# Performance work log

Measured on AMD Instinct MI355X. Metric: run time of the kernel, lower is better.

The kernel has to match this reference:

```python
import jax, jax.numpy as jnp
import numpy as np

NUM_EMBEDDINGS = 8192
EMBEDDING_DIM = 256
COMMITMENT_WEIGHT = 0.25
EMA_DECAY = 0.99
EPSILON = 1e-05


def setup_inputs() -> dict:
    key = jax.random.key(0)
    k1, k2 = jax.random.split(key)
    z = jax.random.normal(k1, (8, 4096, EMBEDDING_DIM), dtype=jnp.float32)
    # xavier-uniform-ish codebook init
    limit = np.sqrt(6.0 / (NUM_EMBEDDINGS + EMBEDDING_DIM))
    embeddings = jax.random.uniform(
        k2, (NUM_EMBEDDINGS, EMBEDDING_DIM), dtype=jnp.float32,
        minval=-limit, maxval=limit)
    ema_cluster_size = jnp.zeros((NUM_EMBEDDINGS,), dtype=jnp.float32)
    ema_embed_sum = embeddings.copy()
    return {
        'z': z,
        'embeddings': embeddings,
        'ema_cluster_size': ema_cluster_size,
        'ema_embed_sum': ema_embed_sum,
    }


def reference(z, embeddings, ema_cluster_size, ema_embed_sum):
    input_shape = z.shape
    D = input_shape[-1]
    z_flat = z.reshape(-1, D)                                  # [N, D]

    # Squared euclidean distances via expansion: ||z||^2 + ||e||^2 - 2 z.e
    z_sq = jnp.sum(z_flat * z_flat, axis=1, keepdims=True)     # [N, 1]
    e_sq = jnp.sum(embeddings * embeddings, axis=1)            # [K]
    ze = jnp.matmul(z_flat, embeddings.T)                      # [N, K]
    distances = z_sq + e_sq - 2.0 * ze                          # [N, K]
    indices = jnp.argmin(distances, axis=1)                    # [N] int

    z_q_flat = embeddings[indices]                             # [N, D] gather
    z_q = z_q_flat.reshape(input_shape)

    # commitment loss = mse(stop_grad(z_q), z)
    diff = jax.lax.stop_gradient(z_q) - z
    commitment_loss = jnp.mean(diff * diff) * COMMITMENT_WEIGHT

    # straight-through estimator
    z_q_st = z + jax.lax.stop_gradient(z_q - z)

    # EMA codebook update (functional version of the in-place buffer update)
    ones = jnp.ones_like(indices, dtype=embeddings.dtype)
    cluster_size = jax.ops.segment_sum(ones, indices, num_segments=NUM_EMBEDDINGS)
    embed_sum = jax.ops.segment_sum(z_flat, indices, num_segments=NUM_EMBEDDINGS)
    new_ema_cluster_size = EMA_DECAY * ema_cluster_size + (1.0 - EMA_DECAY) * cluster_size
    new_ema_embed_sum = EMA_DECAY * ema_embed_sum + (1.0 - EMA_DECAY) * embed_sum
    new_embeddings = new_ema_embed_sum / (new_ema_cluster_size[:, None] + EPSILON)

    indices_out = indices.reshape(input_shape[:-1])
    return (z_q_st, indices_out, commitment_loss,
            new_embeddings, new_ema_cluster_size, new_ema_embed_sum)
```

## Files before the change

### kernel.cpp

```cpp
#include <hip/hip_runtime.h>
#include <hip/hip_bf16.h>
#include <math.h>

#define N_TOK   32768
#define DIM     256
#define KC      8192

#define OUT_ZQ    0
#define OUT_IDX   8388608
#define OUT_LOSS  8421376
#define OUT_NEMB  8421377
#define OUT_CS    10518529
#define OUT_SUM   10526721

#define MARGIN  5e-3f
#define FLAGCAP 8192

typedef __attribute__((ext_vector_type(8))) __bf16 bf16x8;
typedef __attribute__((ext_vector_type(4))) float f32x4;

__device__ __forceinline__ void gload16(const void* g, void* l) {
  __builtin_amdgcn_global_load_lds((const __attribute__((address_space(1))) void*)g,
                                   (__attribute__((address_space(3))) void*)l, 16, 0, 0);
}

__device__ __forceinline__ float np_sumsq256(const float* __restrict__ p, int lane) {
  const int l = lane & 15;
  const int h = l >> 3;
  const int j = l & 7;
  const float* a = p + h * 128 + j;
  float x = a[0];
  float r = __fmul_rn(x, x);
  #pragma unroll
  for (int i = 1; i < 16; ++i) {
    x = a[8 * i];
    r = __fadd_rn(r, __fmul_rn(x, x));
  }
  r = __fadd_rn(r, __shfl_down(r, 1));
  r = __fadd_rn(r, __shfl_down(r, 2));
  r = __fadd_rn(r, __shfl_down(r, 4));
  float hi = __shfl(r, (lane & 48) | 8);
  return __fadd_rn(r, hi);
}

__global__ void vq_prep(const float* __restrict__ emb, float* __restrict__ esq,
                        short* __restrict__ esp2) {
  const int t = threadIdx.x;
  const int code = blockIdx.x * 8 + (t >> 5);
  const int p = t & 31, j = p >> 2, g = p & 3;
  const float* src = emb + (size_t)code * DIM + j * 32 + g * 8;
  const float4 v0 = *(const float4*)src;
  const float4 v1 = *(const float4*)(src + 4);
  const float xf[8] = {v0.x, v0.y, v0.z, v0.w, v1.x, v1.y, v1.z, v1.w};
  bf16x8 hb;
  #pragma unroll
  for (int e = 0; e < 8; ++e) hb[e] = (__bf16)xf[e];
  const int c = code & 15, sub = (code >> 4) & 3, ct = code >> 6;
  const int slot = (g + (c >> 1)) & 3;
  char* dst = (char*)esp2 + (size_t)ct * 32768 + ((sub * 8 + j) << 10) + c * 64 + slot * 16;
  *(bf16x8*)dst = hb;
  if (t < 128) {
    const int code2 = blockIdx.x * 8 + (t >> 4);
    const float s = np_sumsq256(emb + (size_t)code2 * DIM, t & 63);
    if ((t & 15) == 0) esq[code2] = s;
  }
}

__global__ void vq_transpose(const float* __restrict__ emb, float* __restrict__ embT) {
  __shared__ float t[64][65];
  const int tid = threadIdx.x;
  const int bc  = blockIdx.x & 127;
  const int bk  = blockIdx.x >> 7;
  const int cc0 = bc << 6, kc0 = bk << 6;
  const int col = tid & 63, qr = tid >> 6;
  #pragma unroll
  for (int i = 0; i < 16; ++i) {
    const int row = i * 4 + qr;
    t[row][col] = emb[(size_t)(cc0 + row) * DIM + kc0 + col];
  }
  __syncthreads();
  #pragma unroll
  for (int i = 0; i < 16; ++i) {
    const int krow = i * 4 + qr;
    embT[(size_t)(kc0 + krow) * KC + cc0 + col] = t[col][krow];
  }
}

__global__ void vq_init(int* __restrict__ hist, int* __restrict__ cnt) {
  const int i = blockIdx.x * blockDim.x + threadIdx.x;
  hist[i] = 0;
  if (i == 0) cnt[0] = 0;
}

__launch_bounds__(256, 2)
__global__ void vq_mfma(const float* __restrict__ z,
                        const short* __restrict__ esp,
                        const float* __restrict__ esq,
                        float* __restrict__ pb1,
                        int* __restrict__ pi1,
                        float* __restrict__ pb2) {
  __shared__ __align__(16) char lds[65536];
  const int tid  = threadIdx.x;
  const int lane = tid & 63;
  const int w    = tid >> 6;
  const int l15  = lane & 15;
  const int g    = lane >> 4;
  const int rt   = blockIdx.x >> 1;
  const int kh   = blockIdx.x & 1;
  const int row0 = rt * 128 + w * 32;
  const int ct0  = kh * 64, ct1 = ct0 + 64;
  const int gx   = (g + (l15 >> 1)) & 3;
  const char* espb = (const char*)esp;

#define STAGE(CT, BUFB)                                                          \
  {                                                                              \
    _Pragma("unroll")                                                            \
    for (int q_ = 0; q_ < 8; ++q_) {                                             \
      const int so_ = (((w << 3) + q_) << 10) + (lane << 4);                     \
      gload16(espb + (size_t)(CT) * 32768 + so_,                                 \
              (void*)(lds + (BUFB) + (((w << 3) + q_) << 10)));                  \
    }                                                                            \
  }

  STAGE(ct0, 0);

  bf16x8 Ahi[2][8], Alo[2][8];
  #pragma unroll
  for (int s = 0; s < 2; ++s) {
    const float* zr = z + (size_t)(row0 + s * 16 + l15) * DIM + g * 8;
    #pragma unroll
    for (int c = 0; c < 8; ++c) {
      const float4 v0 = *(const float4*)(zr + c * 32);
      const float4 v1 = *(const float4*)(zr + c * 32 + 4);
      const float xf[8] = {v0.x, v0.y, v0.z, v0.w, v1.x, v1.y, v1.z, v1.w};
      #pragma unroll
      for (int e = 0; e < 8; ++e) {
        __bf16 hb = (__bf16)xf[e];
        Ahi[s][c][e] = hb;
        Alo[s][c][e] = (__bf16)(xf[e] - (float)hb);
      }
    }
  }

  __syncthreads();

  float b1[2][4], b2[2][4];
  int   i1[2][4];
  #pragma unroll
  for (int s = 0; s < 2; ++s)
    #pragma unroll
    for (int r = 0; r < 4; ++r) { b1[s][r] = 3.4e38f; b2[s][r] = 3.4e38f; i1[s][r] = 0x7fffffff; }

#define COMP(BUFB)                                                                    \
  {                                                                                   \
    _Pragma("unroll")                                                                 \
    for (int j_ = 0; j_ < 8; ++j_) {                                                  \
      const char* bq_ = lds + (BUFB) + (j_ << 10) + (l15 << 6) + (gx << 4);           \
      const bf16x8 bF0 = *(const bf16x8*)(bq_);                                       \
      const bf16x8 bF1 = *(const bf16x8*)(bq_ + 8192);                                \
      const bf16x8 bF2 = *(const bf16x8*)(bq_ + 16384);                               \
      const bf16x8 bF3 = *(const bf16x8*)(bq_ + 24576);                               \
      acc[0][0] = __builtin_amdgcn_mfma_f32_16x16x32_bf16(Ahi[0][j_], bF0, acc[0][0], 0, 0, 0); \
      acc[0][1] = __builtin_amdgcn_mfma_f32_16x16x32_bf16(Ahi[0][j_], bF1, acc[0][1], 0, 0, 0); \
      acc[0][2] = __builtin_amdgcn_mfma_f32_16x16x32_bf16(Ahi[0][j_], bF2, acc[0][2], 0, 0, 0); \
      acc[0][3] = __builtin_amdgcn_mfma_f32_16x16x32_bf16(Ahi[0][j_], bF3, acc[0][3], 0, 0, 0); \
      acc[1][0] = __builtin_amdgcn_mfma_f32_16x16x32_bf16(Ahi[1][j_], bF0, acc[1][0], 0, 0, 0); \
      acc[1][1] = __builtin_amdgcn_mfma_f32_16x16x32_bf16(Ahi[1][j_], bF1, acc[1][1], 0, 0, 0); \
      acc[1][2] = __builtin_amdgcn_mfma_f32_16x16x32_bf16(Ahi[1][j_], bF2, acc[1][2], 0, 0, 0); \
      acc[1][3] = __builtin_amdgcn_mfma_f32_16x16x32_bf16(Ahi[1][j_], bF3, acc[1][3], 0, 0, 0); \
      acc[0][0] = __builtin_amdgcn_mfma_f32_16x16x32_bf16(Alo[0][j_], bF0, acc[0][0], 0, 0, 0); \
      acc[0][1] = __builtin_amdgcn_mfma_f32_16x16x32_bf16(Alo[0][j_], bF1, acc[0][1], 0, 0, 0); \
      acc[0][2] = __builtin_amdgcn_mfma_f32_16x16x32_bf16(Alo[0][j_], bF2, acc[0][2], 0, 0, 0); \
      acc[0][3] = __builtin_amdgcn_mfma_f32_16x16x32_bf16(Alo[0][j_], bF3, acc[0][3], 0, 0, 0); \
      acc[1][0] = __builtin_amdgcn_mfma_f32_16x16x32_bf16(Alo[1][j_], bF0, acc[1][0], 0, 0, 0); \
      acc[1][1] = __builtin_amdgcn_mfma_f32_16x16x32_bf16(Alo[1][j_], bF1, acc[1][1], 0, 0, 0); \
      acc[1][2] = __builtin_amdgcn_mfma_f32_16x16x32_bf16(Alo[1][j_], bF2, acc[1][2], 0, 0, 0); \
      acc[1][3] = __builtin_amdgcn_mfma_f32_16x16x32_bf16(Alo[1][j_], bF3, acc[1][3], 0, 0, 0); \
    }                                                                                 \
  }

  int bp = 0;
  for (int ct = ct0; ct < ct1; ++ct) {
    if (ct + 1 < ct1) STAGE(ct + 1, (bp ^ 1) << 15);

    float eqv[4];
    #pragma unroll
    for (int sub = 0; sub < 4; ++sub) eqv[sub] = esq[(ct << 6) + sub * 16 + l15];

    f32x4 acc[2][4];
    #pragma unroll
    for (int s = 0; s < 2; ++s)
      #pragma unroll
      for (int sub = 0; sub < 4; ++sub) acc[s][sub] = (f32x4){0.f, 0.f, 0.f, 0.f};

    COMP(bp << 15);

    #pragma unroll
    for (int s = 0; s < 2; ++s) {
      #pragma unroll
      for (int sub = 0; sub < 4; ++sub) {
        const int codeS = (ct << 6) + sub * 16 + l15;
        #pragma unroll
        for (int r = 0; r < 4; ++r) {
          const float sc = fmaf(-2.f, acc[s][sub][r], eqv[sub]);
          const bool lt = sc < b1[s][r];
          b2[s][r] = fminf(b2[s][r], fmaxf(sc, b1[s][r]));
          i1[s][r] = lt ? codeS : i1[s][r];
          b1[s][r] = fminf(b1[s][r], sc);
        }
      }
    }
    __syncthreads();
    bp ^= 1;
  }

  #pragma unroll
  for (int s = 0; s < 2; ++s) {
    #pragma unroll
    for (int r = 0; r < 4; ++r) {
      float v1 = b1[s][r], v2 = b2[s][r];
      int   j1 = i1[s][r];
      #pragma unroll
      for (int off = 1; off < 16; off <<= 1) {
        const float o1 = __shfl_xor(v1, off);
        const int   oj = __shfl_xor(j1, off);
        const float o2 = __shfl_xor(v2, off);
        v2 = fminf(fminf(v2, o2), fmaxf(v1, o1));
        const bool tk = (o1 < v1) || (o1 == v1 && oj < j1);
        j1 = tk ? oj : j1;
        v1 = fminf(v1, o1);
      }
      if (l15 == 0) {
        const int rr = kh * N_TOK + row0 + s * 16 + (g << 2) + r;
        pb1[rr] = v1; pi1[rr] = j1; pb2[rr] = v2;
      }
    }
  }
}

__global__ void vq_merge(const float* __restrict__ pb1, const int* __restrict__ pi1,
                         const float* __restrict__ pb2, int* __restrict__ idxf,
                         int* __restrict__ flag, int* __restrict__ cnt) {
  const int gi = blockIdx.x * blockDim.x + threadIdx.x;
  const float va = pb1[gi],        vb = pb1[N_TOK + gi];
  const int   ia = pi1[gi],        ib = pi1[N_TOK + gi];
  const float v2a = pb2[gi],       v2b = pb2[N_TOK + gi];
  float v1, v2; int i1;
  if (va < vb || (va == vb && ia < ib)) { v1 = va; i1 = ia; v2 = fminf(v2a, vb); }
  else                                  { v1 = vb; i1 = ib; v2 = fminf(v2b, va); }
  idxf[gi] = i1;
  if (v2 - v1 < MARGIN) {
    const int p = atomicAdd(cnt, 1);
    if (p < FLAGCAP) flag[p] = gi;
  }
}

__global__ void vq_rescan2(const float* __restrict__ z,
                           const float* __restrict__ embT,
                           const float* __restrict__ esq,
                           const int* __restrict__ flag,
                           const int* __restrict__ cnt,
                           float* __restrict__ rpv,
                           int* __restrict__ rpi) {
  __shared__ __align__(16) float zT[DIM][16];
  __shared__ float zsq_sh[16];
  __shared__ float rv[4][16];
  __shared__ int   ri[4][16];
  __shared__ int   rown[16];
  int n = *cnt; if (n > FLAGCAP) n = FLAGCAP;
  const int tid = threadIdx.x;
  const int lane = tid & 63, wv = tid >> 6;
  const int nb = (n + 15) >> 4;
  const int ntask = nb * 8;
  for (int task = blockIdx.x; task < ntask; task += gridDim.x) {
    const int bb = task >> 3, cz = task & 7;
    __syncthreads();
    if (tid < 16) rown[tid] = flag[min(bb * 16 + tid, n - 1)];
    __syncthreads();
    #pragma unroll
    for (int rr = 0; rr < 16; ++rr) zT[tid][rr] = z[(size_t)rown[rr] * DIM + tid];
    {
      const int rr = tid >> 4;
      const float s = np_sumsq256(z + (size_t)rown[rr] * DIM, lane);
      if ((tid & 15) == 0) zsq_sh[rr] = s;
    }
    __syncthreads();

    float a[16][4];
    #pragma unroll
    for (int rr = 0; rr < 16; ++rr)
      #pragma unroll
      for (int q = 0; q < 4; ++q) a[rr][q] = 0.f;

    const int c0 = cz * 1024 + tid;
    #pragma unroll 2
    for (int k = 0; k < DIM; ++k) {
      const float* rk = embT + (size_t)k * KC + c0;
      const float e0 = rk[0], e1 = rk[256], e2 = rk[512], e3 = rk[768];
      const f32x4 z0 = *(const f32x4*)&zT[k][0];
      const f32x4 z1 = *(const f32x4*)&zT[k][4];
      const f32x4 z2 = *(const f32x4*)&zT[k][8];
      const f32x4 z3 = *(const f32x4*)&zT[k][12];
      #pragma unroll
      for (int r4 = 0; r4 < 4; ++r4) {
        a[r4][0] = fmaf(z0[r4], e0, a[r4][0]);
        a[r4][1] = fmaf(z0[r4], e1, a[r4][1]);
        a[r4][2] = fmaf(z0[r4], e2, a[r4][2]);
        a[r4][3] = fmaf(z0[r4], e3, a[r4][3]);
        a[4 + r4][0] = fmaf(z1[r4], e0, a[4 + r4][0]);
        a[4 + r4][1] = fmaf(z1[r4], e1, a[4 + r4][1]);
        a[4 + r4][2] = fmaf(z1[r4], e2, a[4 + r4][2]);
        a[4 + r4][3] = fmaf(z1[r4], e3, a[4 + r4][3]);
        a[8 + r4][0] = fmaf(z2[r4], e0, a[8 + r4][0]);
        a[8 + r4][1] = fmaf(z2[r4], e1, a[8 + r4][1]);
        a[8 + r4][2] = fmaf(z2[r4], e2, a[8 + r4][2]);
        a[8 + r4][3] = fmaf(z2[r4], e3, a[8 + r4][3]);
        a[12 + r4][0] = fmaf(z3[r4], e0, a[12 + r4][0]);
        a[12 + r4][1] = fmaf(z3[r4], e1, a[12 + r4][1]);
        a[12 + r4][2] = fmaf(z3[r4], e2, a[12 + r4][2]);
        a[12 + r4][3] = fmaf(z3[r4], e3, a[12 + r4][3]);
      }
    }

    #pragma unroll
    for (int rr = 0; rr < 16; ++rr) {
      float bv = 3.4e38f; int bi = 0x7fffffff;
      #pragma unroll
      for (int q = 0; q < 4; ++q) {
        const int code = cz * 1024 + q * 256 + tid;
        const float D = __fsub_rn(__fadd_rn(zsq_sh[rr], esq[code]), __fmul_rn(2.f, a[rr][q]));
        if (D < bv) { bv = D; bi = code; }
      }
      #pragma unroll
      for (int off = 32; off; off >>= 1) {
        const float ov = __shfl_down(bv, off);
        const int   oi = __shfl_down(bi, off);
        if (ov < bv || (ov == bv && oi < bi)) { bv = ov; bi = oi; }
      }
      if (lane == 0) { rv[wv][rr] = bv; ri[wv][rr] = bi; }
    }
    __syncthreads();
    if (tid < 16) {
      const int fi = bb * 16 + tid;
      if (fi < n) {
        float fv = rv[0][tid]; int fx = ri[0][tid];
        #pragma unroll
        for (int q = 1; q < 4; ++q)
          if (rv[q][tid] < fv || (rv[q][tid] == fv && ri[q][tid] < fx)) { fv = rv[q][tid]; fx = ri[q][tid]; }
        rpv[fi * 8 + cz] = fv; rpi[fi * 8 + cz] = fx;
      }
    }
  }
}

__global__ void vq_rmerge(const int* __restrict__ flag, const int* __restrict__ cnt,
                          const float* __restrict__ rpv, const int* __restrict__ rpi,
                          int* __restrict__ idxf) {
  int n = *cnt; if (n > FLAGCAP) n = FLAGCAP;
  const int fi = blockIdx.x * blockDim.x + threadIdx.x;
  if (fi >= n) return;
  float bv = rpv[fi * 8]; int bi = rpi[fi * 8];
  #pragma unroll
  for (int c = 1; c < 8; ++c) {
    const float v = rpv[fi * 8 + c]; const int ix = rpi[fi * 8 + c];
    if (v < bv || (v == bv && ix < bi)) { bv = v; bi = ix; }
  }
  idxf[flag[fi]] = bi;
}

__global__ void vq_gather(const float* __restrict__ z, const float* __restrict__ emb,
                          const int* __restrict__ idxf, float* __restrict__ out,
                          float* __restrict__ lossp, int* __restrict__ hist) {
  __shared__ float part[4];
  const int tid = threadIdx.x, lane = tid & 63, w = tid >> 6;
  const int row = blockIdx.x * 4 + w;
  const int code = idxf[row];
  const float4 zv = *(const float4*)(z + (size_t)row * DIM + lane * 4);
  const float4 ev = *(const float4*)(emb + (size_t)code * DIM + lane * 4);
  float4 d, o;
  d.x = ev.x - zv.x; d.y = ev.y - zv.y; d.z = ev.z - zv.z; d.w = ev.w - zv.w;
  o.x = zv.x + d.x;  o.y = zv.y + d.y;  o.z = zv.z + d.z;  o.w = zv.w + d.w;
  *(float4*)(out + OUT_ZQ + (size_t)row * DIM + lane * 4) = o;
  float sq = fmaf(d.x, d.x, fmaf(d.y, d.y, fmaf(d.z, d.z, d.w * d.w)));
  #pragma unroll
  for (int off = 32; off; off >>= 1) sq += __shfl_down(sq, off);
  if (lane == 0) {
    part[w] = sq;
    atomicAdd(hist + code, 1);
    out[OUT_IDX + row] = (float)code;
  }
  __syncthreads();
  if (tid == 0) lossp[blockIdx.x] = (part[0] + part[1]) + (part[2] + part[3]);
}

__global__ void vq_prefix(const float* __restrict__ ema_cs, int* __restrict__ hist,
                          int* __restrict__ base, int* __restrict__ cursor,
                          const float* __restrict__ lossp, float* __restrict__ out) {
  __shared__ int ps[256];
  __shared__ float lp[4];
  const int t = threadIdx.x;

  float ls = 0.f;
  #pragma unroll
  for (int j = 0; j < 8; ++j) {
    const float4 v = *(const float4*)(lossp + t * 32 + j * 4);
    ls += (v.x + v.y) + (v.z + v.w);
  }
  #pragma unroll
  for (int off = 32; off; off >>= 1) ls += __shfl_down(ls, off);
  if ((t & 63) == 0) lp[t >> 6] = ls;

  int loc[32]; int s = 0;
  #pragma unroll
  for (int j = 0; j < 32; ++j) { loc[j] = hist[t * 32 + j]; s += loc[j]; }
  ps[t] = s;
  __syncthreads();
  if (t == 0)
    out[OUT_LOSS] = 0.25f * (((lp[0] + lp[1]) + (lp[2] + lp[3])) * (1.f / 8388608.f));
  for (int off = 1; off < 256; off <<= 1) {
    const int v = (t >= off) ? ps[t - off] : 0;
    __syncthreads();
    ps[t] += v;
    __syncthreads();
  }
  int run = ps[t] - s;
  #pragma unroll
  for (int j = 0; j < 32; ++j) {
    const int i = t * 32 + j;
    base[i] = run; cursor[i] = run;
    out[OUT_CS + i] = 0.99f * ema_cs[i] + 0.01f * (float)loc[j];
    run += loc[j];
  }
}

__global__ void vq_slot(const int* __restrict__ idxf, int* __restrict__ cursor,
                        int* __restrict__ rowlist) {
  const int gi = blockIdx.x * blockDim.x + threadIdx.x;
  const int code = idxf[gi];
  const int p = atomicAdd(cursor + code, 1);
  rowlist[p] = gi;
}

__global__ void vq_embsum(const float* __restrict__ z, const float* __restrict__ ema_sum,
                          const int* __restrict__ rowlist, const int* __restrict__ base,
                          const int* __restrict__ hist, float* __restrict__ out) {
  const int code = blockIdx.x;
  const int lane = threadIdx.x;
  const int b = base[code], n = hist[code];
  float a0 = 0.f, a1 = 0.f, a2 = 0.f, a3 = 0.f;
  for (int i = 0; i < n; ++i) {
    const float4 v = *(const float4*)(z + (size_t)rowlist[b + i] * DIM + lane * 4);
    a0 += v.x; a1 += v.y; a2 += v.z; a3 += v.w;
  }
  const float4 es = *(const float4*)(ema_sum + (size_t)code * DIM + lane * 4);
  const float s0 = 0.99f * es.x + 0.01f * a0;
  const float s1 = 0.99f * es.y + 0.01f * a1;
  const float s2 = 0.99f * es.z + 0.01f * a2;
  const float s3 = 0.99f * es.w + 0.01f * a3;
  float* sp = out + OUT_SUM + (size_t)code * DIM + lane * 4;
  sp[0] = s0; sp[1] = s1; sp[2] = s2; sp[3] = s3;
  const float cs = out[OUT_CS + code] + 1e-5f;
  float* np_ = out + OUT_NEMB + (size_t)code * DIM + lane * 4;
  np_[0] = s0 / cs; np_[1] = s1 / cs; np_[2] = s2 / cs; np_[3] = s3 / cs;
}

extern "C" void kernel_launch(void* const* d_in, const int* in_sizes, int n_in,
                              void* d_out, int out_size, void* d_ws, size_t ws_size,
                              hipStream_t stream) {
  const float* z      = (const float*)d_in[0];
  const float* emb    = (const float*)d_in[1];
  const float* emacs  = (const float*)d_in[2];
  const float* emasum = (const float*)d_in[3];
  float* out = (float*)d_out;
  float* ws  = (float*)d_ws;

  float* esq     = ws;
  int*   idxf    = (int*)(ws + 8192);
  int*   flag    = (int*)(ws + 40960);
  int*   cnt     = (int*)(ws + 49152);
  int*   hist    = (int*)(ws + 49408);
  int*   base    = (int*)(ws + 57600);
  int*   cursor  = (int*)(ws + 65792);
  int*   rowlist = (int*)(ws + 73984);
  float* pb1     = ws + 114944;
  int*   pi1     = (int*)(ws + 180480);
  float* pb2     = ws + 246016;
  short* esp2    = (short*)(ws + 311552);
  float* embT    = ws + 1360128;
  float* lossp   = pb1;
  float* rpv     = pb2;
  int*   rpi     = pi1;

  vq_prep<<<KC / 8, 256, 0, stream>>>(emb, esq, esp2);
  vq_transpose<<<512, 256, 0, stream>>>(emb, embT);
  vq_init<<<KC / 256, 256, 0, stream>>>(hist, cnt);

  vq_mfma<<<512, 256, 0, stream>>>(z, esp2, esq, pb1, pi1, pb2);
  vq_merge<<<N_TOK / 256, 256, 0, stream>>>(pb1, pi1, pb2, idxf, flag, cnt);
  vq_rescan2<<<1024, 256, 0, stream>>>(z, embT, esq, flag, cnt, rpv, rpi);
  vq_rmerge<<<FLAGCAP / 256, 256, 0, stream>>>(flag, cnt, rpv, rpi, idxf);

  vq_gather<<<N_TOK / 4, 256, 0, stream>>>(z, emb, idxf, out, lossp, hist);
  vq_prefix<<<1, 256, 0, stream>>>(emacs, hist, base, cursor, lossp, out);
  vq_slot<<<N_TOK / 256, 256, 0, stream>>>(idxf, cursor, rowlist);
  vq_embsum<<<KC, 64, 0, stream>>>(z, emasum, rowlist, base, hist, out);
}
```

Measured before the change: 365.5 us.

## Shrink MFMA distance tile for higher occupancy and widen rescan row batch

The MFMA distance kernel now has each wave handle 16 rows instead of 32 and stage 32 codes per step instead of 64. LDS per block is halved and the launch bound raised to 4 blocks per CU, with the grid doubled to 1024 blocks. The aim is more occupancy and latency hiding, at the cost of less register reuse of each staged codebook tile and more barrier steps. Separately, the fp32 rescan kernel processes 32 flagged rows per task instead of 16, reusing each codebook load across more rows, though this raises register pressure (128 accumulators) and drops the k-loop unroll.

```diff
diff --git a/kernel.cpp b/kernel.cpp
--- a/kernel.cpp
+++ b/kernel.cpp
@@ -92,14 +92,14 @@
   if (i == 0) cnt[0] = 0;
 }
 
-__launch_bounds__(256, 2)
+__launch_bounds__(256, 4)
 __global__ void vq_mfma(const float* __restrict__ z,
                         const short* __restrict__ esp,
                         const float* __restrict__ esq,
                         float* __restrict__ pb1,
                         int* __restrict__ pi1,
                         float* __restrict__ pb2) {
-  __shared__ __align__(16) char lds[65536];
+  __shared__ __align__(16) char lds[32768];
   const int tid  = threadIdx.x;
   const int lane = tid & 63;
   const int w    = tid >> 6;
@@ -107,27 +107,26 @@
   const int g    = lane >> 4;
   const int rt   = blockIdx.x >> 1;
   const int kh   = blockIdx.x & 1;
-  const int row0 = rt * 128 + w * 32;
-  const int ct0  = kh * 64, ct1 = ct0 + 64;
-  const int gx   = (g + (l15 >> 1)) & 3;
+  const int rowbase = rt * 64 + w * 16;
+  const int u0 = kh * 128, u1 = u0 + 128;
+  const int gx = (g + (l15 >> 1)) & 3;
   const char* espb = (const char*)esp;
 
-#define STAGE(CT, BUFB)                                                          \
+#define STAGE(U, BUFB)                                                           \
   {                                                                              \
     _Pragma("unroll")                                                            \
-    for (int q_ = 0; q_ < 8; ++q_) {                                             \
-      const int so_ = (((w << 3) + q_) << 10) + (lane << 4);                     \
-      gload16(espb + (size_t)(CT) * 32768 + so_,                                 \
-              (void*)(lds + (BUFB) + (((w << 3) + q_) << 10)));                  \
+    for (int q_ = 0; q_ < 4; ++q_) {                                             \
+      const int so_ = (((w << 2) + q_) << 10);                                   \
+      gload16(espb + (size_t)(U) * 16384 + so_ + (lane << 4),                    \
+              (void*)(lds + (BUFB) + so_));                                      \
     }                                                                            \
   }
 
-  STAGE(ct0, 0);
-
-  bf16x8 Ahi[2][8], Alo[2][8];
-  #pragma unroll
-  for (int s = 0; s < 2; ++s) {
-    const float* zr = z + (size_t)(row0 + s * 16 + l15) * DIM + g * 8;
+  STAGE(u0, 0);
+
+  bf16x8 Ahi[8], Alo[8];
+  {
+    const float* zr = z + (size_t)(rowbase + l15) * DIM + g * 8;
     #pragma unroll
     for (int c = 0; c < 8; ++c) {
       const float4 v0 = *(const float4*)(zr + c * 32);
@@ -136,104 +135,82 @@
       #pragma unroll
       for (int e = 0; e < 8; ++e) {
         __bf16 hb = (__bf16)xf[e];
-        Ahi[s][c][e] = hb;
-        Alo[s][c][e] = (__bf16)(xf[e] - (float)hb);
+        Ahi[c][e] = hb;
+        Alo[c][e] = (__bf16)(xf[e] - (float)hb);
       }
     }
   }
 
   __syncthreads();
 
-  float b1[2][4], b2[2][4];
-  int   i1[2][4];
-  #pragma unroll
-  for (int s = 0; s < 2; ++s)
-    #pragma unroll
-    for (int r = 0; r < 4; ++r) { b1[s][r] = 3.4e38f; b2[s][r] = 3.4e38f; i1[s][r] = 0x7fffffff; }
-
-#define COMP(BUFB)                                                                    \
-  {                                                                                   \
-    _Pragma("unroll")                                                                 \
-    for (int j_ = 0; j_ < 8; ++j_) {                                                  \
-      const char* bq_ = lds + (BUFB) + (j_ << 10) + (l15 << 6) + (gx << 4);           \
-      const bf16x8 bF0 = *(const bf16x8*)(bq_);                                       \
-      const bf16x8 bF1 = *(const bf16x8*)(bq_ + 8192);                                \
-      const bf16x8 bF2 = *(const bf16x8*)(bq_ + 16384);                               \
-      const bf16x8 bF3 = *(const bf16x8*)(bq_ + 24576);                               \
-      acc[0][0] = __builtin_amdgcn_mfma_f32_16x16x32_bf16(Ahi[0][j_], bF0, acc[0][0], 0, 0, 0); \
-      acc[0][1] = __builtin_amdgcn_mfma_f32_16x16x32_bf16(Ahi[0][j_], bF1, acc[0][1], 0, 0, 0); \
-      acc[0][2] = __builtin_amdgcn_mfma_f32_16x16x32_bf16(Ahi[0][j_], bF2, acc[0][2], 0, 0, 0); \
-      acc[0][3] = __builtin_amdgcn_mfma_f32_16x16x32_bf16(Ahi[0][j_], bF3, acc[0][3], 0, 0, 0); \
-      acc[1][0] = __builtin_amdgcn_mfma_f32_16x16x32_bf16(Ahi[1][j_], bF0, acc[1][0], 0, 0, 0); \
-      acc[1][1] = __builtin_amdgcn_mfma_f32_16x16x32_bf16(Ahi[1][j_], bF1, acc[1][1], 0, 0, 0); \
-      acc[1][2] = __builtin_amdgcn_mfma_f32_16x16x32_bf16(Ahi[1][j_], bF2, acc[1][2], 0, 0, 0); \
-      acc[1][3] = __builtin_amdgcn_mfma_f32_16x16x32_bf16(Ahi[1][j_], bF3, acc[1][3], 0, 0, 0); \
-      acc[0][0] = __builtin_amdgcn_mfma_f32_16x16x32_bf16(Alo[0][j_], bF0, acc[0][0], 0, 0, 0); \
-      acc[0][1] = __builtin_amdgcn_mfma_f32_16x16x32_bf16(Alo[0][j_], bF1, acc[0][1], 0, 0, 0); \
-      acc[0][2] = __builtin_amdgcn_mfma_f32_16x16x32_bf16(Alo[0][j_], bF2, acc[0][2], 0, 0, 0); \
-      acc[0][3] = __builtin_amdgcn_mfma_f32_16x16x32_bf16(Alo[0][j_], bF3, acc[0][3], 0, 0, 0); \
-      acc[1][0] = __builtin_amdgcn_mfma_f32_16x16x32_bf16(Alo[1][j_], bF0, acc[1][0], 0, 0, 0); \
-      acc[1][1] = __builtin_amdgcn_mfma_f32_16x16x32_bf16(Alo[1][j_], bF1, acc[1][1], 0, 0, 0); \
-      acc[1][2] = __builtin_amdgcn_mfma_f32_16x16x32_bf16(Alo[1][j_], bF2, acc[1][2], 0, 0, 0); \
-      acc[1][3] = __builtin_amdgcn_mfma_f32_16x16x32_bf16(Alo[1][j_], bF3, acc[1][3], 0, 0, 0); \
-    }                                                                                 \
-  }
+  float b1[4], b2[4];
+  int   i1[4];
+  #pragma unroll
+  for (int r = 0; r < 4; ++r) { b1[r] = 3.4e38f; b2[r] = 3.4e38f; i1[r] = 0x7fffffff; }
 
   int bp = 0;
-  for (int ct = ct0; ct < ct1; ++ct) {
-    if (ct + 1 < ct1) STAGE(ct + 1, (bp ^ 1) << 15);
-
-    float eqv[4];
-    #pragma unroll
-    for (int sub = 0; sub < 4; ++sub) eqv[sub] = esq[(ct << 6) + sub * 16 + l15];
-
-    f32x4 acc[2][4];
-    #pragma unroll
-    for (int s = 0; s < 2; ++s)
-      #pragma unroll
-      for (int sub = 0; sub < 4; ++sub) acc[s][sub] = (f32x4){0.f, 0.f, 0.f, 0.f};
-
-    COMP(bp << 15);
-
-    #pragma unroll
-    for (int s = 0; s < 2; ++s) {
-      #pragma unroll
-      for (int sub = 0; sub < 4; ++sub) {
-        const int codeS = (ct << 6) + sub * 16 + l15;
-        #pragma unroll
-        for (int r = 0; r < 4; ++r) {
-          const float sc = fmaf(-2.f, acc[s][sub][r], eqv[sub]);
-          const bool lt = sc < b1[s][r];
-          b2[s][r] = fminf(b2[s][r], fmaxf(sc, b1[s][r]));
-          i1[s][r] = lt ? codeS : i1[s][r];
-          b1[s][r] = fminf(b1[s][r], sc);
-        }
-      }
+  for (int u = u0; u < u1; ++u) {
+    if (u + 1 < u1) STAGE(u + 1, (bp ^ 1) << 14);
+
+    const float eq0 = esq[(u << 5) + l15];
+    const float eq1 = esq[(u << 5) + 16 + l15];
+
+    f32x4 acc0 = (f32x4){0.f, 0.f, 0.f, 0.f};
+    f32x4 acc1 = (f32x4){0.f, 0.f, 0.f, 0.f};
+
+    {
+      const char* base = lds + (bp << 14);
+      #pragma unroll
+      for (int j_ = 0; j_ < 8; ++j_) {
+        const char* bq_ = base + (j_ << 10) + (l15 << 6) + (gx << 4);
+        const bf16x8 bF0 = *(const bf16x8*)(bq_);
+        const bf16x8 bF1 = *(const bf16x8*)(bq_ + 8192);
+        acc0 = __builtin_amdgcn_mfma_f32_16x16x32_bf16(Ahi[j_], bF0, acc0, 0, 0, 0);
+        acc1 = __builtin_amdgcn_mfma_f32_16x16x32_bf16(Ahi[j_], bF1, acc1, 0, 0, 0);
+        acc0 = __builtin_amdgcn_mfma_f32_16x16x32_bf16(Alo[j_], bF0, acc0, 0, 0, 0);
+        acc1 = __builtin_amdgcn_mfma_f32_16x16x32_bf16(Alo[j_], bF1, acc1, 0, 0, 0);
+      }
+    }
+
+    const int code0 = (u << 5) + l15;
+    #pragma unroll
+    for (int r = 0; r < 4; ++r) {
+      const float sc = fmaf(-2.f, acc0[r], eq0);
+      const bool lt = sc < b1[r];
+      b2[r] = fminf(b2[r], fmaxf(sc, b1[r]));
+      i1[r] = lt ? code0 : i1[r];
+      b1[r] = fminf(b1[r], sc);
+    }
+    const int code1 = code0 + 16;
+    #pragma unroll
+    for (int r = 0; r < 4; ++r) {
+      const float sc = fmaf(-2.f, acc1[r], eq1);
+      const bool lt = sc < b1[r];
+      b2[r] = fminf(b2[r], fmaxf(sc, b1[r]));
+      i1[r] = lt ? code1 : i1[r];
+      b1[r] = fminf(b1[r], sc);
     }
     __syncthreads();
     bp ^= 1;
   }
 
   #pragma unroll
-  for (int s = 0; s < 2; ++s) {
-    #pragma unroll
-    for (int r = 0; r < 4; ++r) {
-      float v1 = b1[s][r], v2 = b2[s][r];
-      int   j1 = i1[s][r];
-      #pragma unroll
-      for (int off = 1; off < 16; off <<= 1) {
-        const float o1 = __shfl_xor(v1, off);
-        const int   oj = __shfl_xor(j1, off);
-        const float o2 = __shfl_xor(v2, off);
-        v2 = fminf(fminf(v2, o2), fmaxf(v1, o1));
-        const bool tk = (o1 < v1) || (o1 == v1 && oj < j1);
-        j1 = tk ? oj : j1;
-        v1 = fminf(v1, o1);
-      }
-      if (l15 == 0) {
-        const int rr = kh * N_TOK + row0 + s * 16 + (g << 2) + r;
-        pb1[rr] = v1; pi1[rr] = j1; pb2[rr] = v2;
-      }
+  for (int r = 0; r < 4; ++r) {
+    float v1 = b1[r], v2 = b2[r];
+    int   j1 = i1[r];
+    #pragma unroll
+    for (int off = 1; off < 16; off <<= 1) {
+      const float o1 = __shfl_xor(v1, off);
+      const int   oj = __shfl_xor(j1, off);
+      const float o2 = __shfl_xor(v2, off);
+      v2 = fminf(fminf(v2, o2), fmaxf(v1, o1));
+      const bool tk = (o1 < v1) || (o1 == v1 && oj < j1);
+      j1 = tk ? oj : j1;
+      v1 = fminf(v1, o1);
+    }
+    if (l15 == 0) {
+      const int rr = kh * N_TOK + rowbase + (g << 2) + r;
+      pb1[rr] = v1; pi1[rr] = j1; pb2[rr] = v2;
     }
   }
 }
@@ -262,68 +239,57 @@
                            const int* __restrict__ cnt,
                            float* __restrict__ rpv,
                            int* __restrict__ rpi) {
-  __shared__ __align__(16) float zT[DIM][16];
-  __shared__ float zsq_sh[16];
-  __shared__ float rv[4][16];
-  __shared__ int   ri[4][16];
-  __shared__ int   rown[16];
+  __shared__ __align__(16) float zT[DIM][32];
+  __shared__ float zsq_sh[32];
+  __shared__ float rv[4][32];
+  __shared__ int   ri[4][32];
+  __shared__ int   rown[32];
   int n = *cnt; if (n > FLAGCAP) n = FLAGCAP;
   const int tid = threadIdx.x;
   const int lane = tid & 63, wv = tid >> 6;
-  const int nb = (n + 15) >> 4;
+  const int nb = (n + 31) >> 5;
   const int ntask = nb * 8;
   for (int task = blockIdx.x; task < ntask; task += gridDim.x) {
     const int bb = task >> 3, cz = task & 7;
     __syncthreads();
-    if (tid < 16) rown[tid] = flag[min(bb * 16 + tid, n - 1)];
-    __syncthreads();
-    #pragma unroll
-    for (int rr = 0; rr < 16; ++rr) zT[tid][rr] = z[(size_t)rown[rr] * DIM + tid];
-    {
-      const int rr = tid >> 4;
-      const float s = np_sumsq256(z + (size_t)rown[rr] * DIM, lane);
+    if (tid < 32) rown[tid] = flag[min(bb * 32 + tid, n - 1)];
+    __syncthreads();
+    #pragma unroll
+    for (int rr = 0; rr < 32; ++rr) zT[tid][rr] = z[(size_t)rown[rr] * DIM + tid];
+    #pragma unroll
+    for (int h = 0; h < 2; ++h) {
+      const int rr = h * 16 + (tid >> 4);
+      const float s = np_sumsq256(z + (size_t)rown[rr] * DIM, tid & 63);
       if ((tid & 15) == 0) zsq_sh[rr] = s;
     }
     __syncthreads();
 
-    float a[16][4];
-    #pragma unroll
-    for (int rr = 0; rr < 16; ++rr)
+    float a[32][4];
+    #pragma unroll
+    for (int rr = 0; rr < 32; ++rr)
       #pragma unroll
       for (int q = 0; q < 4; ++q) a[rr][q] = 0.f;
 
     const int c0 = cz * 1024 + tid;
-    #pragma unroll 2
+    #pragma unroll 1
     for (int k = 0; k < DIM; ++k) {
       const float* rk = embT + (size_t)k * KC + c0;
       const float e0 = rk[0], e1 = rk[256], e2 = rk[512], e3 = rk[768];
-      const f32x4 z0 = *(const f32x4*)&zT[k][0];
-      const f32x4 z1 = *(const f32x4*)&zT[k][4];
-      const f32x4 z2 = *(const f32x4*)&zT[k][8];
-      const f32x4 z3 = *(const f32x4*)&zT[k][12];
-      #pragma unroll
-      for (int r4 = 0; r4 < 4; ++r4) {
-        a[r4][0] = fmaf(z0[r4], e0, a[r4][0]);
-        a[r4][1] = fmaf(z0[r4], e1, a[r4][1]);
-        a[r4][2] = fmaf(z0[r4], e2, a[r4][2]);
-        a[r4][3] = fmaf(z0[r4], e3, a[r4][3]);
-        a[4 + r4][0] = fmaf(z1[r4], e0, a[4 + r4][0]);
-        a[4 + r4][1] = fmaf(z1[r4], e1, a[4 + r4][1]);
-        a[4 + r4][2] = fmaf(z1[r4], e2, a[4 + r4][2]);
-        a[4 + r4][3] = fmaf(z1[r4], e3, a[4 + r4][3]);
-        a[8 + r4][0] = fmaf(z2[r4], e0, a[8 + r4][0]);
-        a[8 + r4][1] = fmaf(z2[r4], e1, a[8 + r4][1]);
-        a[8 + r4][2] = fmaf(z2[r4], e2, a[8 + r4][2]);
-        a[8 + r4][3] = fmaf(z2[r4], e3, a[8 + r4][3]);
-        a[12 + r4][0] = fmaf(z3[r4], e0, a[12 + r4][0]);
-        a[12 + r4][1] = fmaf(z3[r4], e1, a[12 + r4][1]);
-        a[12 + r4][2] = fmaf(z3[r4], e2, a[12 + r4][2]);
-        a[12 + r4][3] = fmaf(z3[r4], e3, a[12 + r4][3]);
-      }
-    }
-
-    #pragma unroll
-    for (int rr = 0; rr < 16; ++rr) {
+      #pragma unroll
+      for (int h = 0; h < 8; ++h) {
+        const f32x4 zv = *(const f32x4*)&zT[k][h * 4];
+        #pragma unroll
+        for (int r4 = 0; r4 < 4; ++r4) {
+          a[h * 4 + r4][0] = fmaf(zv[r4], e0, a[h * 4 + r4][0]);
+          a[h * 4 + r4][1] = fmaf(zv[r4], e1, a[h * 4 + r4][1]);
+          a[h * 4 + r4][2] = fmaf(zv[r4], e2, a[h * 4 + r4][2]);
+          a[h * 4 + r4][3] = fmaf(zv[r4], e3, a[h * 4 + r4][3]);
+        }
+      }
+    }
+
+    #pragma unroll
+    for (int rr = 0; rr < 32; ++rr) {
       float bv = 3.4e38f; int bi = 0x7fffffff;
       #pragma unroll
       for (int q = 0; q < 4; ++q) {
@@ -340,8 +306,8 @@
       if (lane == 0) { rv[wv][rr] = bv; ri[wv][rr] = bi; }
     }
     __syncthreads();
-    if (tid < 16) {
-      const int fi = bb * 16 + tid;
+    if (tid < 32) {
+      const int fi = bb * 32 + tid;
       if (fi < n) {
         float fv = rv[0][tid]; int fx = ri[0][tid];
         #pragma unroll
@@ -495,7 +461,7 @@
   vq_transpose<<<512, 256, 0, stream>>>(emb, embT);
   vq_init<<<KC / 256, 256, 0, stream>>>(hist, cnt);
 
-  vq_mfma<<<512, 256, 0, stream>>>(z, esp2, esq, pb1, pi1, pb2);
+  vq_mfma<<<1024, 256, 0, stream>>>(z, esp2, esq, pb1, pi1, pb2);
   vq_merge<<<N_TOK / 256, 256, 0, stream>>>(pb1, pi1, pb2, idxf, flag, cnt);
   vq_rescan2<<<1024, 256, 0, stream>>>(z, embT, esq, flag, cnt, rpv, rpi);
   vq_rmerge<<<FLAGCAP / 256, 256, 0, stream>>>(flag, cnt, rpv, rpi, idxf);
```

Result: slower. 1.092 ms (+198.8%).
